# Optimization experiments

Measured on AMD Instinct MI355X. Metric: run time of the kernel, lower is better.

Reference implementation:

```python
import jax, jax.numpy as jnp
import numpy as np

M = 200000   # number of lane candidates
N = 5000     # number of obstacles
NUM_NODE = 150
FEAT = 4


def setup_inputs() -> dict:
    key = jax.random.key(0)
    k1, k2, k3 = jax.random.split(key, 3)
    lane_features = jax.random.normal(k1, (M, NUM_NODE, FEAT), dtype=jnp.float32)
    obs_pos = jax.random.normal(k2, (N, 2), dtype=jnp.float32)
    same_obs_mask = jnp.sort(jax.random.randint(k3, (M, 1), 0, N), axis=0)
    return {"lane_features": lane_features, "obs_pos": obs_pos,
            "same_obs_mask": same_obs_mask}


def reference(lane_features, obs_pos, same_obs_mask):
    lf = lane_features.astype(jnp.float32)          # (M, 150, 4)
    m = lf.shape[0]
    ar = jnp.arange(m)

    # BroadcastObstaclesToLanes: the serial masked-write loop is exactly a gather.
    rep = obs_pos[same_obs_mask[:, 0]].astype(jnp.float32)   # (M, 2)

    # FindClosestNodeFromLineToPoint: interior nodes [1:-1], xy only.
    nodes = lf[:, 1:-1, :2]                          # (M, 148, 2)
    dists = jnp.sum((nodes - rep[:, None, :]) ** 2, axis=-1)  # (M, 148)
    min_idx = jnp.argmin(dists, axis=1) + 1          # (M,), in [1, 148]

    # FindClosestLineSegmentFromLineToPoint (note: distances use all 4 feats,
    # faithfully matching line_nodes[..., :] in the original).
    min_node = lf[ar, min_idx]                       # (M, 4)
    node_prev = lf[ar, min_idx - 1]
    node_next = lf[ar, min_idx + 1]
    dist_prev = jnp.sum((node_prev - min_node) ** 2, axis=1)
    dist_next = jnp.sum((node_next - min_node) ** 2, axis=1)
    min_idx_2nd = jnp.where(dist_next < dist_prev, min_idx + 1, min_idx - 1)
    idx_before = jnp.minimum(min_idx, min_idx_2nd)
    idx_after = jnp.maximum(min_idx, min_idx_2nd)

    # PointToLineProjection on the xy of the chosen segment endpoints.
    seg_s = lf[ar, idx_before, :2]                   # (M, 2)
    seg_e = lf[ar, idx_after, :2]                    # (M, 2)
    line_vec = seg_e - seg_s
    mag = jnp.sqrt(jnp.sum(line_vec ** 2, axis=1, keepdims=True))
    unit = line_vec / mag
    proj_mag = jnp.sum((rep - seg_s) * unit, axis=1, keepdims=True)
    proj_pt = seg_s + proj_mag * unit                # (M, 2)

    indices = jnp.stack([idx_before, idx_after], axis=1)  # (M, 2)
    return proj_pt, indices, rep
```

## Files before the change

### kernel.cpp

```cpp
#include <hip/hip_runtime.h>
#include <math.h>

static constexpr int M_ROWS   = 200000;
static constexpr int NUM_NODE = 150;
static constexpr int ROWS_PER_BLOCK = 4;

__global__ __launch_bounds__(256) void obstacle_to_lane_kernel(
    const float* __restrict__ lf,
    const float* __restrict__ obs_pos,
    const int*   __restrict__ mask,
    float*       __restrict__ out)
{
    const int wave = threadIdx.x >> 6;
    const int lane = threadIdx.x & 63;
    const int m = blockIdx.x * ROWS_PER_BLOCK + wave;
    if (m >= M_ROWS) return;

    const float* row = lf + (size_t)m * (NUM_NODE * 4);

    const int obs_idx = mask[m];
    const float rx = obs_pos[2 * obs_idx];
    const float ry = obs_pos[2 * obs_idx + 1];

    float best_d = INFINITY;
    int   best_j = 1 << 30;
    #pragma unroll
    for (int r = 0; r < 3; ++r) {
        const int j = 1 + lane + r * 64;
        if (j <= NUM_NODE - 2) {
            const float4 n = *reinterpret_cast<const float4*>(row + 4 * j);
            const float dx = __fsub_rn(n.x, rx);
            const float dy = __fsub_rn(n.y, ry);
            const float d  = __fadd_rn(__fmul_rn(dx, dx), __fmul_rn(dy, dy));
            if (d < best_d) { best_d = d; best_j = j; }
        }
    }
    #pragma unroll
    for (int off = 32; off > 0; off >>= 1) {
        const float od = __shfl_down(best_d, off, 64);
        const int   oj = __shfl_down(best_j, off, 64);
        if (od < best_d || (od == best_d && oj < best_j)) { best_d = od; best_j = oj; }
    }
    const int min_idx = __shfl(best_j, 0, 64);

    if (lane == 0) {
        const float4 a = *reinterpret_cast<const float4*>(row + 4 * (min_idx - 1));
        const float4 c = *reinterpret_cast<const float4*>(row + 4 * min_idx);
        const float4 b = *reinterpret_cast<const float4*>(row + 4 * (min_idx + 1));

        float t, s;
        t = __fsub_rn(a.x, c.x); s = __fmul_rn(t, t);
        t = __fsub_rn(a.y, c.y); s = __fadd_rn(s, __fmul_rn(t, t));
        t = __fsub_rn(a.z, c.z); s = __fadd_rn(s, __fmul_rn(t, t));
        t = __fsub_rn(a.w, c.w); s = __fadd_rn(s, __fmul_rn(t, t));
        const float dist_prev = s;
        t = __fsub_rn(b.x, c.x); s = __fmul_rn(t, t);
        t = __fsub_rn(b.y, c.y); s = __fadd_rn(s, __fmul_rn(t, t));
        t = __fsub_rn(b.z, c.z); s = __fadd_rn(s, __fmul_rn(t, t));
        t = __fsub_rn(b.w, c.w); s = __fadd_rn(s, __fmul_rn(t, t));
        const float dist_next = s;

        float sx, sy, ex, ey;
        int ib;
        if (dist_next < dist_prev) {
            ib = min_idx;     sx = c.x; sy = c.y; ex = b.x; ey = b.y;
        } else {
            ib = min_idx - 1; sx = a.x; sy = a.y; ex = c.x; ey = c.y;
        }

        const float lvx = __fsub_rn(ex, sx);
        const float lvy = __fsub_rn(ey, sy);
        const float mag = __fsqrt_rn(__fadd_rn(__fmul_rn(lvx, lvx), __fmul_rn(lvy, lvy)));
        const float ux  = __fdiv_rn(lvx, mag);
        const float uy  = __fdiv_rn(lvy, mag);
        const float pm  = __fadd_rn(__fmul_rn(__fsub_rn(rx, sx), ux),
                                    __fmul_rn(__fsub_rn(ry, sy), uy));
        const float px  = __fadd_rn(sx, __fmul_rn(pm, ux));
        const float py  = __fadd_rn(sy, __fmul_rn(pm, uy));

        float* o_proj = out + 2 * (size_t)m;
        o_proj[0] = px; o_proj[1] = py;
        float* o_idx = out + 2 * (size_t)M_ROWS + 2 * (size_t)m;
        o_idx[0] = (float)ib; o_idx[1] = (float)(ib + 1);
        float* o_rep = out + 4 * (size_t)M_ROWS + 2 * (size_t)m;
        o_rep[0] = rx; o_rep[1] = ry;
    }
}

extern "C" void kernel_launch(void* const* d_in, const int* in_sizes, int n_in,
                              void* d_out, int out_size, void* d_ws, size_t ws_size,
                              hipStream_t stream) {
    const float* lf      = (const float*)d_in[0];
    const float* obs_pos = (const float*)d_in[1];
    const int*   mask    = (const int*)d_in[2];
    float*       out     = (float*)d_out;

    const int grid = (M_ROWS + ROWS_PER_BLOCK - 1) / ROWS_PER_BLOCK;
    hipLaunchKernelGGL(obstacle_to_lane_kernel, dim3(grid), dim3(256), 0, stream,
                       lf, obs_pos, mask, out);
}
```

Before: 612.8 us.

## Use persistent waves with software-prefetched rows and shuffle-based neighbour fetch

Replaces the one-row-per-wave launch with a fixed grid of 2048 blocks. Each wave now processes a contiguous range of rows and prefetches the next row's nodes and obstacle position while it computes the current one. The whole row, including the endpoint nodes, is loaded into registers, so the neighbour nodes come from lane shuffles instead of a second dependent global load. The three outputs are written as float2 stores spread across three lanes. The goal is to hide memory latency on a bandwidth-bound streaming kernel, at the cost of more registers per thread and a fixed grid size.

Measured after the change: 649.1 us. 5.9% more time.

```diff
diff --git a/kernel.cpp b/kernel.cpp
--- a/kernel.cpp
+++ b/kernel.cpp
@@ -3,9 +3,12 @@
 
 static constexpr int M_ROWS   = 200000;
 static constexpr int NUM_NODE = 150;
-static constexpr int ROWS_PER_BLOCK = 4;
+static constexpr int ROW_F    = NUM_NODE * 4;
+static constexpr int BLOCKS   = 2048;
+static constexpr int WPB      = 4;
+static constexpr int TOTAL_WAVES = BLOCKS * WPB;
 
-__global__ __launch_bounds__(256) void obstacle_to_lane_kernel(
+__global__ __launch_bounds__(256, 6) void obstacle_to_lane_kernel(
     const float* __restrict__ lf,
     const float* __restrict__ obs_pos,
     const int*   __restrict__ mask,
@@ -13,59 +16,96 @@
 {
     const int wave = threadIdx.x >> 6;
     const int lane = threadIdx.x & 63;
-    const int m = blockIdx.x * ROWS_PER_BLOCK + wave;
-    if (m >= M_ROWS) return;
+    const int wid  = blockIdx.x * WPB + wave;
 
-    const float* row = lf + (size_t)m * (NUM_NODE * 4);
+    const int base = M_ROWS / TOTAL_WAVES;
+    const int rem  = M_ROWS % TOTAL_WAVES;
+    const int m0   = wid * base + (wid < rem ? wid : rem);
+    const int m1   = m0 + base + (wid < rem ? 1 : 0);
 
-    const int obs_idx = mask[m];
-    const float rx = obs_pos[2 * obs_idx];
-    const float ry = obs_pos[2 * obs_idx + 1];
+    const int  j0   = lane;
+    const int  j1   = lane + 64;
+    const int  j2c  = (lane + 128 <= NUM_NODE - 1) ? (lane + 128) : (NUM_NODE - 1);
+    const bool amin0 = (j0 >= 1);
+    const bool amin2 = (lane + 128 <= NUM_NODE - 2);
 
-    float best_d = INFINITY;
-    int   best_j = 1 << 30;
-    #pragma unroll
-    for (int r = 0; r < 3; ++r) {
-        const int j = 1 + lane + r * 64;
-        if (j <= NUM_NODE - 2) {
-            const float4 n = *reinterpret_cast<const float4*>(row + 4 * j);
-            const float dx = __fsub_rn(n.x, rx);
-            const float dy = __fsub_rn(n.y, ry);
-            const float d  = __fadd_rn(__fmul_rn(dx, dx), __fmul_rn(dy, dy));
-            if (d < best_d) { best_d = d; best_j = j; }
+    const float* row = lf + (size_t)m0 * ROW_F;
+
+    float4 c0 = *reinterpret_cast<const float4*>(row + 4 * j0);
+    float4 c1 = *reinterpret_cast<const float4*>(row + 4 * j1);
+    float4 c2 = *reinterpret_cast<const float4*>(row + 4 * j2c);
+    int obs0 = mask[m0];
+    float rx = obs_pos[2 * obs0];
+    float ry = obs_pos[2 * obs0 + 1];
+
+    for (int m = m0; m < m1; ++m) {
+        float4 n0, n1, n2;
+        float nrx, nry;
+        const bool has_next = (m + 1 < m1);
+        if (has_next) {
+            const float* nrow = row + ROW_F;
+            n0 = *reinterpret_cast<const float4*>(nrow + 4 * j0);
+            n1 = *reinterpret_cast<const float4*>(nrow + 4 * j1);
+            n2 = *reinterpret_cast<const float4*>(nrow + 4 * j2c);
+            const int nobs = mask[m + 1];
+            nrx = obs_pos[2 * nobs];
+            nry = obs_pos[2 * nobs + 1];
         }
-    }
-    #pragma unroll
-    for (int off = 32; off > 0; off >>= 1) {
-        const float od = __shfl_down(best_d, off, 64);
-        const int   oj = __shfl_down(best_j, off, 64);
-        if (od < best_d || (od == best_d && oj < best_j)) { best_d = od; best_j = oj; }
-    }
-    const int min_idx = __shfl(best_j, 0, 64);
 
-    if (lane == 0) {
-        const float4 a = *reinterpret_cast<const float4*>(row + 4 * (min_idx - 1));
-        const float4 c = *reinterpret_cast<const float4*>(row + 4 * min_idx);
-        const float4 b = *reinterpret_cast<const float4*>(row + 4 * (min_idx + 1));
+        float best_d = INFINITY;
+        int   best_j = 1 << 30;
+        {
+            float dx = __fsub_rn(c0.x, rx), dy = __fsub_rn(c0.y, ry);
+            float d  = __fadd_rn(__fmul_rn(dx, dx), __fmul_rn(dy, dy));
+            if (amin0 && d < best_d) { best_d = d; best_j = j0; }
+            dx = __fsub_rn(c1.x, rx); dy = __fsub_rn(c1.y, ry);
+            d  = __fadd_rn(__fmul_rn(dx, dx), __fmul_rn(dy, dy));
+            if (d < best_d) { best_d = d; best_j = j1; }
+            dx = __fsub_rn(c2.x, rx); dy = __fsub_rn(c2.y, ry);
+            d  = __fadd_rn(__fmul_rn(dx, dx), __fmul_rn(dy, dy));
+            if (amin2 && d < best_d) { best_d = d; best_j = lane + 128; }
+        }
+        #pragma unroll
+        for (int off = 32; off > 0; off >>= 1) {
+            const float od = __shfl_down(best_d, off, 64);
+            const int   oj = __shfl_down(best_j, off, 64);
+            if (od < best_d || (od == best_d && oj < best_j)) { best_d = od; best_j = oj; }
+        }
+        const int min_idx = __shfl(best_j, 0, 64);
+
+        auto pick = [&](int q) -> float4 {
+            const int sl = q & 63;
+            const int rr = q >> 6;
+            const float4 s = (rr == 0) ? c0 : ((rr == 1) ? c1 : c2);
+            float4 r;
+            r.x = __shfl(s.x, sl, 64);
+            r.y = __shfl(s.y, sl, 64);
+            r.z = __shfl(s.z, sl, 64);
+            r.w = __shfl(s.w, sl, 64);
+            return r;
+        };
+        const float4 na = pick(min_idx - 1);
+        const float4 nc = pick(min_idx);
+        const float4 nb = pick(min_idx + 1);
 
         float t, s;
-        t = __fsub_rn(a.x, c.x); s = __fmul_rn(t, t);
-        t = __fsub_rn(a.y, c.y); s = __fadd_rn(s, __fmul_rn(t, t));
-        t = __fsub_rn(a.z, c.z); s = __fadd_rn(s, __fmul_rn(t, t));
-        t = __fsub_rn(a.w, c.w); s = __fadd_rn(s, __fmul_rn(t, t));
+        t = __fsub_rn(na.x, nc.x); s = __fmul_rn(t, t);
+        t = __fsub_rn(na.y, nc.y); s = __fadd_rn(s, __fmul_rn(t, t));
+        t = __fsub_rn(na.z, nc.z); s = __fadd_rn(s, __fmul_rn(t, t));
+        t = __fsub_rn(na.w, nc.w); s = __fadd_rn(s, __fmul_rn(t, t));
         const float dist_prev = s;
-        t = __fsub_rn(b.x, c.x); s = __fmul_rn(t, t);
-        t = __fsub_rn(b.y, c.y); s = __fadd_rn(s, __fmul_rn(t, t));
-        t = __fsub_rn(b.z, c.z); s = __fadd_rn(s, __fmul_rn(t, t));
-        t = __fsub_rn(b.w, c.w); s = __fadd_rn(s, __fmul_rn(t, t));
+        t = __fsub_rn(nb.x, nc.x); s = __fmul_rn(t, t);
+        t = __fsub_rn(nb.y, nc.y); s = __fadd_rn(s, __fmul_rn(t, t));
+        t = __fsub_rn(nb.z, nc.z); s = __fadd_rn(s, __fmul_rn(t, t));
+        t = __fsub_rn(nb.w, nc.w); s = __fadd_rn(s, __fmul_rn(t, t));
         const float dist_next = s;
 
         float sx, sy, ex, ey;
         int ib;
         if (dist_next < dist_prev) {
-            ib = min_idx;     sx = c.x; sy = c.y; ex = b.x; ey = b.y;
+            ib = min_idx;     sx = nc.x; sy = nc.y; ex = nb.x; ey = nb.y;
         } else {
-            ib = min_idx - 1; sx = a.x; sy = a.y; ex = c.x; ey = c.y;
+            ib = min_idx - 1; sx = na.x; sy = na.y; ex = nc.x; ey = nc.y;
         }
 
         const float lvx = __fsub_rn(ex, sx);
@@ -78,12 +118,27 @@
         const float px  = __fadd_rn(sx, __fmul_rn(pm, ux));
         const float py  = __fadd_rn(sy, __fmul_rn(pm, uy));
 
-        float* o_proj = out + 2 * (size_t)m;
-        o_proj[0] = px; o_proj[1] = py;
-        float* o_idx = out + 2 * (size_t)M_ROWS + 2 * (size_t)m;
-        o_idx[0] = (float)ib; o_idx[1] = (float)(ib + 1);
-        float* o_rep = out + 4 * (size_t)M_ROWS + 2 * (size_t)m;
-        o_rep[0] = rx; o_rep[1] = ry;
+        if (lane < 3) {
+            float2 v;
+            size_t off;
+            if (lane == 0) {
+                v = make_float2(px, py);
+                off = 2 * (size_t)m;
+            } else if (lane == 1) {
+                v = make_float2((float)ib, (float)(ib + 1));
+                off = 2 * (size_t)M_ROWS + 2 * (size_t)m;
+            } else {
+                v = make_float2(rx, ry);
+                off = 4 * (size_t)M_ROWS + 2 * (size_t)m;
+            }
+            *reinterpret_cast<float2*>(out + off) = v;
+        }
+
+        if (has_next) {
+            row += ROW_F;
+            c0 = n0; c1 = n1; c2 = n2;
+            rx = nrx; ry = nry;
+        }
     }
 }
 
@@ -95,7 +150,6 @@
     const int*   mask    = (const int*)d_in[2];
     float*       out     = (float*)d_out;
 
-    const int grid = (M_ROWS + ROWS_PER_BLOCK - 1) / ROWS_PER_BLOCK;
-    hipLaunchKernelGGL(obstacle_to_lane_kernel, dim3(grid), dim3(256), 0, stream,
+    hipLaunchKernelGGL(obstacle_to_lane_kernel, dim3(BLOCKS), dim3(256), 0, stream,
                        lf, obs_pos, mask, out);
 }
```

## Stage row groups through double-buffered LDS in persistent blocks with shuffle neighbor fetch

Applied to the files above, without the earlier changes.

Replaces the one-wave-per-row launch with a fixed grid of 2500 persistent blocks. Each block loops over groups of 16 rows, copying each group into a double-buffered shared-memory tile while computing on the previous one. Neighbor nodes are read with wave shuffles instead of extra global loads by lane 0, and outputs are written as float2 by three lanes. This aims to hide global memory latency and coalesce the streaming read. In exchange it uses about 77 KB of shared memory per block, which limits occupancy, and the copy-then-compute path may not overlap well since the stage writes are synchronous.

Measured after the change: 722.6 us. +17.9%, slower.

```diff
diff --git a/kernel.cpp b/kernel.cpp
--- a/kernel.cpp
+++ b/kernel.cpp
@@ -3,7 +3,13 @@
 
 static constexpr int M_ROWS   = 200000;
 static constexpr int NUM_NODE = 150;
-static constexpr int ROWS_PER_BLOCK = 4;
+static constexpr int ROW_F4   = NUM_NODE;
+static constexpr int RPG      = 16;
+static constexpr int GROUPS   = M_ROWS / RPG;
+static constexpr int GRID     = 2500;
+static constexpr int GPB      = GROUPS / GRID;
+static constexpr int F4_PER_GROUP = RPG * ROW_F4;
+static constexpr int THREADS  = 256;
 
 __global__ __launch_bounds__(256) void obstacle_to_lane_kernel(
     const float* __restrict__ lf,
@@ -11,79 +17,124 @@
     const int*   __restrict__ mask,
     float*       __restrict__ out)
 {
-    const int wave = threadIdx.x >> 6;
-    const int lane = threadIdx.x & 63;
-    const int m = blockIdx.x * ROWS_PER_BLOCK + wave;
-    if (m >= M_ROWS) return;
+    __shared__ float4 sbuf[2][F4_PER_GROUP];
+    __shared__ int    smask[2][RPG];
 
-    const float* row = lf + (size_t)m * (NUM_NODE * 4);
+    const int tid  = threadIdx.x;
+    const int wave = tid >> 6;
+    const int lane = tid & 63;
 
-    const int obs_idx = mask[m];
-    const float rx = obs_pos[2 * obs_idx];
-    const float ry = obs_pos[2 * obs_idx + 1];
+    auto stage = [&](int buf, int grp) {
+        const float4* src = reinterpret_cast<const float4*>(lf) + (size_t)grp * F4_PER_GROUP;
+        #pragma unroll
+        for (int k = 0; k < 10; ++k) {
+            const int idx = tid + k * THREADS;
+            if (idx < F4_PER_GROUP) sbuf[buf][idx] = src[idx];
+        }
+        if (tid < RPG) smask[buf][tid] = mask[grp * RPG + tid];
+    };
 
-    float best_d = INFINITY;
-    int   best_j = 1 << 30;
-    #pragma unroll
-    for (int r = 0; r < 3; ++r) {
-        const int j = 1 + lane + r * 64;
-        if (j <= NUM_NODE - 2) {
-            const float4 n = *reinterpret_cast<const float4*>(row + 4 * j);
-            const float dx = __fsub_rn(n.x, rx);
-            const float dy = __fsub_rn(n.y, ry);
-            const float d  = __fadd_rn(__fmul_rn(dx, dx), __fmul_rn(dy, dy));
-            if (d < best_d) { best_d = d; best_j = j; }
+    auto compute = [&](int buf, int grp) {
+        #pragma unroll 1
+        for (int rr = 0; rr < RPG / 4; ++rr) {
+            const int r = wave * (RPG / 4) + rr;
+            const int m = grp * RPG + r;
+
+            const int o  = smask[buf][r];
+            const float rx = obs_pos[2 * o];
+            const float ry = obs_pos[2 * o + 1];
+
+            const float4* row = &sbuf[buf][r * ROW_F4];
+            const float4 c0 = row[lane];
+            const float4 c1 = row[lane + 64];
+            const float4 c2 = row[(lane + 128 < NUM_NODE) ? (lane + 128) : (NUM_NODE - 1)];
+
+            float best_d = INFINITY;
+            int   best_j = 1 << 30;
+            {
+                float dx, dy, d;
+                dx = __fsub_rn(c0.x, rx); dy = __fsub_rn(c0.y, ry);
+                d  = __fadd_rn(__fmul_rn(dx, dx), __fmul_rn(dy, dy));
+                if (lane >= 1 && d < best_d) { best_d = d; best_j = lane; }
+                dx = __fsub_rn(c1.x, rx); dy = __fsub_rn(c1.y, ry);
+                d  = __fadd_rn(__fmul_rn(dx, dx), __fmul_rn(dy, dy));
+                if (d < best_d) { best_d = d; best_j = lane + 64; }
+                dx = __fsub_rn(c2.x, rx); dy = __fsub_rn(c2.y, ry);
+                d  = __fadd_rn(__fmul_rn(dx, dx), __fmul_rn(dy, dy));
+                if (lane + 128 <= NUM_NODE - 2 && d < best_d) { best_d = d; best_j = lane + 128; }
+            }
+            #pragma unroll
+            for (int off = 32; off > 0; off >>= 1) {
+                const float od = __shfl_down(best_d, off, 64);
+                const int   oj = __shfl_down(best_j, off, 64);
+                if (od < best_d || (od == best_d && oj < best_j)) { best_d = od; best_j = oj; }
+            }
+            const int min_idx = __shfl(best_j, 0, 64);
+
+            auto pick = [&](int q) -> float4 {
+                const int sl = q & 63;
+                const int g  = q >> 6;
+                const float4 s = (g == 0) ? c0 : ((g == 1) ? c1 : c2);
+                float4 res;
+                res.x = __shfl(s.x, sl, 64);
+                res.y = __shfl(s.y, sl, 64);
+                res.z = __shfl(s.z, sl, 64);
+                res.w = __shfl(s.w, sl, 64);
+                return res;
+            };
+            const float4 na = pick(min_idx - 1);
+            const float4 nc = pick(min_idx);
+            const float4 nb = pick(min_idx + 1);
+
+            float t, s;
+            t = __fsub_rn(na.x, nc.x); s = __fmul_rn(t, t);
+            t = __fsub_rn(na.y, nc.y); s = __fadd_rn(s, __fmul_rn(t, t));
+            t = __fsub_rn(na.z, nc.z); s = __fadd_rn(s, __fmul_rn(t, t));
+            t = __fsub_rn(na.w, nc.w); s = __fadd_rn(s, __fmul_rn(t, t));
+            const float dist_prev = s;
+            t = __fsub_rn(nb.x, nc.x); s = __fmul_rn(t, t);
+            t = __fsub_rn(nb.y, nc.y); s = __fadd_rn(s, __fmul_rn(t, t));
+            t = __fsub_rn(nb.z, nc.z); s = __fadd_rn(s, __fmul_rn(t, t));
+            t = __fsub_rn(nb.w, nc.w); s = __fadd_rn(s, __fmul_rn(t, t));
+            const float dist_next = s;
+
+            float sx, sy, ex, ey;
+            int ib;
+            if (dist_next < dist_prev) {
+                ib = min_idx;     sx = nc.x; sy = nc.y; ex = nb.x; ey = nb.y;
+            } else {
+                ib = min_idx - 1; sx = na.x; sy = na.y; ex = nc.x; ey = nc.y;
+            }
+
+            const float lvx = __fsub_rn(ex, sx);
+            const float lvy = __fsub_rn(ey, sy);
+            const float mag = __fsqrt_rn(__fadd_rn(__fmul_rn(lvx, lvx), __fmul_rn(lvy, lvy)));
+            const float ux  = __fdiv_rn(lvx, mag);
+            const float uy  = __fdiv_rn(lvy, mag);
+            const float pm  = __fadd_rn(__fmul_rn(__fsub_rn(rx, sx), ux),
+                                        __fmul_rn(__fsub_rn(ry, sy), uy));
+            const float px  = __fadd_rn(sx, __fmul_rn(pm, ux));
+            const float py  = __fadd_rn(sy, __fmul_rn(pm, uy));
+
+            if (lane < 3) {
+                float2 v; size_t off;
+                if (lane == 0)      { v = make_float2(px, py);                        off = 2 * (size_t)m; }
+                else if (lane == 1) { v = make_float2((float)ib, (float)(ib + 1));    off = 2 * (size_t)M_ROWS + 2 * (size_t)m; }
+                else                { v = make_float2(rx, ry);                        off = 4 * (size_t)M_ROWS + 2 * (size_t)m; }
+                *reinterpret_cast<float2*>(out + off) = v;
+            }
         }
-    }
-    #pragma unroll
-    for (int off = 32; off > 0; off >>= 1) {
-        const float od = __shfl_down(best_d, off, 64);
-        const int   oj = __shfl_down(best_j, off, 64);
-        if (od < best_d || (od == best_d && oj < best_j)) { best_d = od; best_j = oj; }
-    }
-    const int min_idx = __shfl(best_j, 0, 64);
+    };
 
-    if (lane == 0) {
-        const float4 a = *reinterpret_cast<const float4*>(row + 4 * (min_idx - 1));
-        const float4 c = *reinterpret_cast<const float4*>(row + 4 * min_idx);
-        const float4 b = *reinterpret_cast<const float4*>(row + 4 * (min_idx + 1));
-
-        float t, s;
-        t = __fsub_rn(a.x, c.x); s = __fmul_rn(t, t);
-        t = __fsub_rn(a.y, c.y); s = __fadd_rn(s, __fmul_rn(t, t));
-        t = __fsub_rn(a.z, c.z); s = __fadd_rn(s, __fmul_rn(t, t));
-        t = __fsub_rn(a.w, c.w); s = __fadd_rn(s, __fmul_rn(t, t));
-        const float dist_prev = s;
-        t = __fsub_rn(b.x, c.x); s = __fmul_rn(t, t);
-        t = __fsub_rn(b.y, c.y); s = __fadd_rn(s, __fmul_rn(t, t));
-        t = __fsub_rn(b.z, c.z); s = __fadd_rn(s, __fmul_rn(t, t));
-        t = __fsub_rn(b.w, c.w); s = __fadd_rn(s, __fmul_rn(t, t));
-        const float dist_next = s;
-
-        float sx, sy, ex, ey;
-        int ib;
-        if (dist_next < dist_prev) {
-            ib = min_idx;     sx = c.x; sy = c.y; ex = b.x; ey = b.y;
-        } else {
-            ib = min_idx - 1; sx = a.x; sy = a.y; ex = c.x; ey = c.y;
-        }
-
-        const float lvx = __fsub_rn(ex, sx);
-        const float lvy = __fsub_rn(ey, sy);
-        const float mag = __fsqrt_rn(__fadd_rn(__fmul_rn(lvx, lvx), __fmul_rn(lvy, lvy)));
-        const float ux  = __fdiv_rn(lvx, mag);
-        const float uy  = __fdiv_rn(lvy, mag);
-        const float pm  = __fadd_rn(__fmul_rn(__fsub_rn(rx, sx), ux),
-                                    __fmul_rn(__fsub_rn(ry, sy), uy));
-        const float px  = __fadd_rn(sx, __fmul_rn(pm, ux));
-        const float py  = __fadd_rn(sy, __fmul_rn(pm, uy));
-
-        float* o_proj = out + 2 * (size_t)m;
-        o_proj[0] = px; o_proj[1] = py;
-        float* o_idx = out + 2 * (size_t)M_ROWS + 2 * (size_t)m;
-        o_idx[0] = (float)ib; o_idx[1] = (float)(ib + 1);
-        float* o_rep = out + 4 * (size_t)M_ROWS + 2 * (size_t)m;
-        o_rep[0] = rx; o_rep[1] = ry;
+    const int g0 = blockIdx.x;
+    stage(0, g0);
+    int cur = 0;
+    #pragma unroll 1
+    for (int i = 0; i < GPB; ++i) {
+        __syncthreads();
+        if (i + 1 < GPB) stage(cur ^ 1, g0 + (i + 1) * GRID);
+        compute(cur, g0 + i * GRID);
+        cur ^= 1;
     }
 }
 
@@ -95,7 +146,6 @@
     const int*   mask    = (const int*)d_in[2];
     float*       out     = (float*)d_out;
 
-    const int grid = (M_ROWS + ROWS_PER_BLOCK - 1) / ROWS_PER_BLOCK;
-    hipLaunchKernelGGL(obstacle_to_lane_kernel, dim3(grid), dim3(256), 0, stream,
+    hipLaunchKernelGGL(obstacle_to_lane_kernel, dim3(GRID), dim3(THREADS), 0, stream,
                        lf, obs_pos, mask, out);
 }
```

## Process six rows per wave with batched float2 loads and interleaved reductions

Applied to the files above, without the earlier changes.

Each wave now handles six lane rows instead of one. All node xy loads for those rows are issued up front as float2 reads rather than float4, which gives more memory-level parallelism per wave. The six argmin shuffle reductions are interleaved, and the three outputs are written as float2 stores spread over lanes 0-2. The grid shrinks sixfold and register use rises, which may lower occupancy, and the float2 loads still touch the same cache lines as before.

Measured after the change: 626.7 us. +2.3%, slower.

```diff
diff --git a/kernel.cpp b/kernel.cpp
--- a/kernel.cpp
+++ b/kernel.cpp
@@ -3,7 +3,10 @@
 
 static constexpr int M_ROWS   = 200000;
 static constexpr int NUM_NODE = 150;
-static constexpr int ROWS_PER_BLOCK = 4;
+static constexpr int ROW_F    = NUM_NODE * 4;
+static constexpr int RPW      = 6;
+static constexpr int RPB      = 4 * RPW;
+static constexpr int GRID     = (M_ROWS + RPB - 1) / RPB;
 
 __global__ __launch_bounds__(256) void obstacle_to_lane_kernel(
     const float* __restrict__ lf,
@@ -13,77 +16,113 @@
 {
     const int wave = threadIdx.x >> 6;
     const int lane = threadIdx.x & 63;
-    const int m = blockIdx.x * ROWS_PER_BLOCK + wave;
-    if (m >= M_ROWS) return;
+    const int m0   = blockIdx.x * RPB + wave * RPW;
 
-    const float* row = lf + (size_t)m * (NUM_NODE * 4);
+    int nrows = M_ROWS - m0;
+    if (nrows <= 0) return;
+    if (nrows > RPW) nrows = RPW;
 
-    const int obs_idx = mask[m];
-    const float rx = obs_pos[2 * obs_idx];
-    const float ry = obs_pos[2 * obs_idx + 1];
+    const int  j0   = lane;
+    const int  j1   = lane + 64;
+    const int  j2   = lane + 128;
+    const int  j2c  = (j2 < NUM_NODE) ? j2 : (NUM_NODE - 1);
+    const bool a0ok = (lane >= 1);
+    const bool a2ok = (j2 <= NUM_NODE - 2);
 
-    float best_d = INFINITY;
-    int   best_j = 1 << 30;
+    float2 q0[RPW], q1[RPW], q2[RPW];
+    float  rx[RPW], ry[RPW];
     #pragma unroll
-    for (int r = 0; r < 3; ++r) {
-        const int j = 1 + lane + r * 64;
-        if (j <= NUM_NODE - 2) {
-            const float4 n = *reinterpret_cast<const float4*>(row + 4 * j);
-            const float dx = __fsub_rn(n.x, rx);
-            const float dy = __fsub_rn(n.y, ry);
-            const float d  = __fadd_rn(__fmul_rn(dx, dx), __fmul_rn(dy, dy));
-            if (d < best_d) { best_d = d; best_j = j; }
+    for (int r = 0; r < RPW; ++r) {
+        if (r < nrows) {
+            const float* row = lf + (size_t)(m0 + r) * ROW_F;
+            q0[r] = *reinterpret_cast<const float2*>(row + 4 * j0);
+            q1[r] = *reinterpret_cast<const float2*>(row + 4 * j1);
+            q2[r] = *reinterpret_cast<const float2*>(row + 4 * j2c);
+            const int o = mask[m0 + r];
+            rx[r] = obs_pos[2 * o];
+            ry[r] = obs_pos[2 * o + 1];
         }
     }
+
+    float bd[RPW];
+    int   bj[RPW];
+    #pragma unroll
+    for (int r = 0; r < RPW; ++r) {
+        bd[r] = INFINITY;
+        bj[r] = 1 << 30;
+        if (r < nrows) {
+            float dx, dy, d;
+            dx = __fsub_rn(q0[r].x, rx[r]); dy = __fsub_rn(q0[r].y, ry[r]);
+            d  = __fadd_rn(__fmul_rn(dx, dx), __fmul_rn(dy, dy));
+            if (a0ok && d < bd[r]) { bd[r] = d; bj[r] = j0; }
+            dx = __fsub_rn(q1[r].x, rx[r]); dy = __fsub_rn(q1[r].y, ry[r]);
+            d  = __fadd_rn(__fmul_rn(dx, dx), __fmul_rn(dy, dy));
+            if (d < bd[r]) { bd[r] = d; bj[r] = j1; }
+            dx = __fsub_rn(q2[r].x, rx[r]); dy = __fsub_rn(q2[r].y, ry[r]);
+            d  = __fadd_rn(__fmul_rn(dx, dx), __fmul_rn(dy, dy));
+            if (a2ok && d < bd[r]) { bd[r] = d; bj[r] = j2; }
+        }
+    }
+
     #pragma unroll
     for (int off = 32; off > 0; off >>= 1) {
-        const float od = __shfl_down(best_d, off, 64);
-        const int   oj = __shfl_down(best_j, off, 64);
-        if (od < best_d || (od == best_d && oj < best_j)) { best_d = od; best_j = oj; }
+        #pragma unroll
+        for (int r = 0; r < RPW; ++r) {
+            const float od = __shfl_down(bd[r], off, 64);
+            const int   oj = __shfl_down(bj[r], off, 64);
+            if (od < bd[r] || (od == bd[r] && oj < bj[r])) { bd[r] = od; bj[r] = oj; }
+        }
     }
-    const int min_idx = __shfl(best_j, 0, 64);
 
-    if (lane == 0) {
-        const float4 a = *reinterpret_cast<const float4*>(row + 4 * (min_idx - 1));
-        const float4 c = *reinterpret_cast<const float4*>(row + 4 * min_idx);
-        const float4 b = *reinterpret_cast<const float4*>(row + 4 * (min_idx + 1));
+    #pragma unroll
+    for (int r = 0; r < RPW; ++r) {
+        if (r < nrows) {
+            const int m       = m0 + r;
+            const int min_idx = __shfl(bj[r], 0, 64);
+            const float* row  = lf + (size_t)m * ROW_F;
 
-        float t, s;
-        t = __fsub_rn(a.x, c.x); s = __fmul_rn(t, t);
-        t = __fsub_rn(a.y, c.y); s = __fadd_rn(s, __fmul_rn(t, t));
-        t = __fsub_rn(a.z, c.z); s = __fadd_rn(s, __fmul_rn(t, t));
-        t = __fsub_rn(a.w, c.w); s = __fadd_rn(s, __fmul_rn(t, t));
-        const float dist_prev = s;
-        t = __fsub_rn(b.x, c.x); s = __fmul_rn(t, t);
-        t = __fsub_rn(b.y, c.y); s = __fadd_rn(s, __fmul_rn(t, t));
-        t = __fsub_rn(b.z, c.z); s = __fadd_rn(s, __fmul_rn(t, t));
-        t = __fsub_rn(b.w, c.w); s = __fadd_rn(s, __fmul_rn(t, t));
-        const float dist_next = s;
+            const float4 a = *reinterpret_cast<const float4*>(row + 4 * (min_idx - 1));
+            const float4 c = *reinterpret_cast<const float4*>(row + 4 * min_idx);
+            const float4 b = *reinterpret_cast<const float4*>(row + 4 * (min_idx + 1));
 
-        float sx, sy, ex, ey;
-        int ib;
-        if (dist_next < dist_prev) {
-            ib = min_idx;     sx = c.x; sy = c.y; ex = b.x; ey = b.y;
-        } else {
-            ib = min_idx - 1; sx = a.x; sy = a.y; ex = c.x; ey = c.y;
+            float t, s;
+            t = __fsub_rn(a.x, c.x); s = __fmul_rn(t, t);
+            t = __fsub_rn(a.y, c.y); s = __fadd_rn(s, __fmul_rn(t, t));
+            t = __fsub_rn(a.z, c.z); s = __fadd_rn(s, __fmul_rn(t, t));
+            t = __fsub_rn(a.w, c.w); s = __fadd_rn(s, __fmul_rn(t, t));
+            const float dist_prev = s;
+            t = __fsub_rn(b.x, c.x); s = __fmul_rn(t, t);
+            t = __fsub_rn(b.y, c.y); s = __fadd_rn(s, __fmul_rn(t, t));
+            t = __fsub_rn(b.z, c.z); s = __fadd_rn(s, __fmul_rn(t, t));
+            t = __fsub_rn(b.w, c.w); s = __fadd_rn(s, __fmul_rn(t, t));
+            const float dist_next = s;
+
+            float sx, sy, ex, ey;
+            int ib;
+            if (dist_next < dist_prev) {
+                ib = min_idx;     sx = c.x; sy = c.y; ex = b.x; ey = b.y;
+            } else {
+                ib = min_idx - 1; sx = a.x; sy = a.y; ex = c.x; ey = c.y;
+            }
+
+            const float lvx = __fsub_rn(ex, sx);
+            const float lvy = __fsub_rn(ey, sy);
+            const float mag = __fsqrt_rn(__fadd_rn(__fmul_rn(lvx, lvx), __fmul_rn(lvy, lvy)));
+            const float ux  = __fdiv_rn(lvx, mag);
+            const float uy  = __fdiv_rn(lvy, mag);
+            const float pm  = __fadd_rn(__fmul_rn(__fsub_rn(rx[r], sx), ux),
+                                        __fmul_rn(__fsub_rn(ry[r], sy), uy));
+            const float px  = __fadd_rn(sx, __fmul_rn(pm, ux));
+            const float py  = __fadd_rn(sy, __fmul_rn(pm, uy));
+
+            if (lane < 3) {
+                float2 v; size_t off;
+                if (lane == 0)      { v = make_float2(px, py);                     off = 2 * (size_t)m; }
+                else if (lane == 1) { v = make_float2((float)ib, (float)(ib + 1)); off = 2 * (size_t)M_ROWS + 2 * (size_t)m; }
+                else                { v = make_float2(rx[r], ry[r]);               off = 4 * (size_t)M_ROWS + 2 * (size_t)m; }
+                *reinterpret_cast<float2*>(out + off) = v;
+            }
         }
-
-        const float lvx = __fsub_rn(ex, sx);
-        const float lvy = __fsub_rn(ey, sy);
-        const float mag = __fsqrt_rn(__fadd_rn(__fmul_rn(lvx, lvx), __fmul_rn(lvy, lvy)));
-        const float ux  = __fdiv_rn(lvx, mag);
-        const float uy  = __fdiv_rn(lvy, mag);
-        const float pm  = __fadd_rn(__fmul_rn(__fsub_rn(rx, sx), ux),
-                                    __fmul_rn(__fsub_rn(ry, sy), uy));
-        const float px  = __fadd_rn(sx, __fmul_rn(pm, ux));
-        const float py  = __fadd_rn(sy, __fmul_rn(pm, uy));
-
-        float* o_proj = out + 2 * (size_t)m;
-        o_proj[0] = px; o_proj[1] = py;
-        float* o_idx = out + 2 * (size_t)M_ROWS + 2 * (size_t)m;
-        o_idx[0] = (float)ib; o_idx[1] = (float)(ib + 1);
-        float* o_rep = out + 4 * (size_t)M_ROWS + 2 * (size_t)m;
-        o_rep[0] = rx; o_rep[1] = ry;
     }
 }
 
@@ -95,7 +134,6 @@
     const int*   mask    = (const int*)d_in[2];
     float*       out     = (float*)d_out;
 
-    const int grid = (M_ROWS + ROWS_PER_BLOCK - 1) / ROWS_PER_BLOCK;
-    hipLaunchKernelGGL(obstacle_to_lane_kernel, dim3(grid), dim3(256), 0, stream,
+    hipLaunchKernelGGL(obstacle_to_lane_kernel, dim3(GRID), dim3(256), 0, stream,
                        lf, obs_pos, mask, out);
 }
```
